# Kernel optimization log

Hardware: AMD Instinct MI355X
Metric: run time of the kernel (lower is better)

The kernel has to match this reference:

```python
import jax, jax.numpy as jnp
import numpy as np

# Model dims (Llama-7B-like with GQA)
HID = 4096      # hidden_size
NH = 32         # query heads
NKV = 8         # kv heads
D = HID // NH   # head_dim = 128
S = 64          # num decode sequences (one token each)
NB = 4096       # num cache blocks
BS = 16         # block size
MC = 1024       # max context length
THETA = 10000.0 # rope base


def _rope(x, positions):
    # x: [S, h, D]; neox-style rotary over full head_dim
    half = D // 2
    inv_freq = 1.0 / (THETA ** (jnp.arange(half, dtype=jnp.float32) * 2.0 / D))
    ang = positions.astype(jnp.float32)[:, None] * inv_freq  # [S, half]
    cos = jnp.cos(ang)[:, None, :]
    sin = jnp.sin(ang)[:, None, :]
    x1, x2 = x[..., :half], x[..., half:]
    return jnp.concatenate([x1 * cos - x2 * sin, x2 * cos + x1 * sin], axis=-1)


def setup_inputs() -> dict:
    key = jax.random.key(0)
    ks = jax.random.split(key, 8)
    hidden_states = jax.random.normal(ks[0], (S, HID), dtype=jnp.float32)
    k_cache = jax.random.normal(ks[1], (NB, BS, NKV, D), dtype=jnp.float32)
    v_cache = jax.random.normal(ks[2], (NB, BS, NKV, D), dtype=jnp.float32)
    qkv_w = jax.random.normal(ks[3], ((NH + 2 * NKV) * D, HID), dtype=jnp.float32) * 0.02
    o_w = jax.random.normal(ks[4], (HID, NH * D), dtype=jnp.float32) * 0.02
    context_lens = jnp.clip(jax.random.randint(ks[5], (S,), 1, MC + 1), 1, MC).astype(jnp.int32)
    positions = (context_lens - 1).astype(jnp.int32)  # current token position
    block_tables = jax.random.randint(ks[6], (S, MC // BS), 0, NB).astype(jnp.int32)
    return {"hidden_states": hidden_states, "k_cache": k_cache, "v_cache": v_cache,
            "qkv_w": qkv_w, "o_w": o_w, "positions": positions,
            "context_lens": context_lens, "block_tables": block_tables}


def reference(hidden_states, k_cache, v_cache, qkv_w, o_w, positions, context_lens, block_tables):
    # QKV projection (no bias)
    qkv = hidden_states @ qkv_w.T  # [S, (NH+2*NKV)*D]
    q, k, v = jnp.split(qkv, [NH * D, NH * D + NKV * D], axis=-1)
    q = _rope(q.reshape(S, NH, D), positions)
    k = _rope(k.reshape(S, NKV, D), positions)
    v = v.reshape(S, NKV, D)

    # paged KV gather via block tables: [S, MC, NKV, D]
    Kg = k_cache[block_tables].reshape(S, MC, NKV, D)
    Vg = v_cache[block_tables].reshape(S, MC, NKV, D)
    # write current token's k/v into its slot (positions = context_len - 1)
    idx = jnp.arange(S)
    Kg = Kg.at[idx, positions].set(k)
    Vg = Vg.at[idx, positions].set(v)

    # GQA attention without expanding KV heads
    G = NH // NKV
    qh = q.reshape(S, NKV, G, D) * (D ** -0.5)
    scores = jnp.einsum('skgd,sckd->skgc', qh, Kg)  # [S, NKV, G, MC]
    mask = jnp.arange(MC)[None, :] < context_lens[:, None]  # [S, MC]
    scores = jnp.where(mask[:, None, None, :], scores, -1e9)
    probs = jax.nn.softmax(scores, axis=-1)
    attn = jnp.einsum('skgc,sckd->skgd', probs, Vg).reshape(S, NH * D)

    # output projection
    return attn @ o_w.T
```

## Files before the change

### kernel.cpp

```cpp
#include <hip/hip_runtime.h>
#include <math.h>

#define HID 4096
#define NH  32
#define NKV 8
#define DH  128
#define SEQ 64
#define BS  16
#define MC  1024
#define QKV_N 6144
#define NPAGES 64
#define KC  64
#define KS  16
#define GQ  4
#define CSPLIT 8
#define TPS 128
#define RT  32
#define NHQ (SEQ * NH)
#define SCALE 0.08838834764831845f

__device__ float g_qkv[SEQ * QKV_N];
__device__ float g_attn[SEQ * HID];
__device__ float g_part[KS * SEQ * QKV_N];
__device__ float g_po[CSPLIT * NHQ * DH];
__device__ float g_pm[CSPLIT * NHQ];
__device__ float g_pl[CSPLIT * NHQ];

__global__ __launch_bounds__(256) void gemm_tile(const float* __restrict__ X,
                                                 const float* __restrict__ W,
                                                 float* __restrict__ P,
                                                 int N, int K) {
    __shared__ float Xs[KC][68];
    __shared__ float Ws[KC][68];
    const int tid = threadIdx.x;
    const int tx = tid & 15;
    const int ty = tid >> 4;
    const int jb = blockIdx.x * 64;
    const int ks = blockIdx.y;
    const int k_lo = ks * (K / KS);
    const int k_hi = k_lo + (K / KS);

    float4 a0 = {0,0,0,0}, a1 = {0,0,0,0}, a2 = {0,0,0,0}, a3 = {0,0,0,0};

    for (int k0 = k_lo; k0 < k_hi; k0 += KC) {
        #pragma unroll
        for (int r = 0; r < 4; ++r) {
            int idx = r * 256 + tid;
            int s  = idx >> 4;
            int k4 = idx & 15;
            float4 v = *(const float4*)(X + (size_t)s * K + k0 + k4 * 4);
            Xs[k4 * 4 + 0][s] = v.x;
            Xs[k4 * 4 + 1][s] = v.y;
            Xs[k4 * 4 + 2][s] = v.z;
            Xs[k4 * 4 + 3][s] = v.w;
        }
        #pragma unroll
        for (int r = 0; r < 4; ++r) {
            int idx = r * 256 + tid;
            int j  = idx >> 4;
            int k4 = idx & 15;
            float4 v = *(const float4*)(W + (size_t)(jb + j) * K + k0 + k4 * 4);
            Ws[k4 * 4 + 0][j] = v.x;
            Ws[k4 * 4 + 1][j] = v.y;
            Ws[k4 * 4 + 2][j] = v.z;
            Ws[k4 * 4 + 3][j] = v.w;
        }
        __syncthreads();
        #pragma unroll
        for (int kk = 0; kk < KC; ++kk) {
            float4 xv = *(const float4*)(&Xs[kk][ty * 4]);
            float4 wv = *(const float4*)(&Ws[kk][tx * 4]);
            a0.x = fmaf(xv.x, wv.x, a0.x); a0.y = fmaf(xv.x, wv.y, a0.y);
            a0.z = fmaf(xv.x, wv.z, a0.z); a0.w = fmaf(xv.x, wv.w, a0.w);
            a1.x = fmaf(xv.y, wv.x, a1.x); a1.y = fmaf(xv.y, wv.y, a1.y);
            a1.z = fmaf(xv.y, wv.z, a1.z); a1.w = fmaf(xv.y, wv.w, a1.w);
            a2.x = fmaf(xv.z, wv.x, a2.x); a2.y = fmaf(xv.z, wv.y, a2.y);
            a2.z = fmaf(xv.z, wv.z, a2.z); a2.w = fmaf(xv.z, wv.w, a2.w);
            a3.x = fmaf(xv.w, wv.x, a3.x); a3.y = fmaf(xv.w, wv.y, a3.y);
            a3.z = fmaf(xv.w, wv.z, a3.z); a3.w = fmaf(xv.w, wv.w, a3.w);
        }
        __syncthreads();
    }
    float* pb = P + (size_t)ks * SEQ * N;
    *(float4*)(pb + (size_t)(ty * 4 + 0) * N + jb + tx * 4) = a0;
    *(float4*)(pb + (size_t)(ty * 4 + 1) * N + jb + tx * 4) = a1;
    *(float4*)(pb + (size_t)(ty * 4 + 2) * N + jb + tx * 4) = a2;
    *(float4*)(pb + (size_t)(ty * 4 + 3) * N + jb + tx * 4) = a3;
}

__global__ __launch_bounds__(256) void reduce_ks(const float* __restrict__ P,
                                                 float* __restrict__ Y, int n4) {
    int t = blockIdx.x * 256 + threadIdx.x;
    if (t >= n4) return;
    const float4* p4 = (const float4*)P;
    float4 r = p4[t];
    #pragma unroll
    for (int i = 1; i < KS; ++i) {
        float4 v = p4[t + (size_t)i * n4];
        r.x += v.x; r.y += v.y; r.z += v.z; r.w += v.w;
    }
    ((float4*)Y)[t] = r;
}

__global__ __launch_bounds__(256) void rope_scalar(float* __restrict__ qkv,
                                                   const int* __restrict__ ia,
                                                   const int* __restrict__ ib) {
    int t = blockIdx.x * 256 + threadIdx.x;
    if (t >= SEQ * (NH + NKV) * 64) return;
    int i = t & 63;
    int h = (t >> 6) % (NH + NKV);
    int s = t / ((NH + NKV) * 64);
    int pos = max(ia[s], ib[s]) - 1;
    float* base = qkv + (size_t)s * QKV_N + (size_t)h * DH;
    float ang = (float)pos / powf(10000.0f, (float)i * 2.0f / (float)DH);
    float sn, c;
    sincosf(ang, &sn, &c);
    float x1 = base[i];
    float x2 = base[i + 64];
    base[i]      = x1 * c - x2 * sn;
    base[i + 64] = x2 * c + x1 * sn;
}

__global__ __launch_bounds__(256) void attn_reg(const float* __restrict__ qkv,
                                                const float* __restrict__ k_cache,
                                                const float* __restrict__ v_cache,
                                                const int* __restrict__ ia,
                                                const int* __restrict__ ib,
                                                const int* __restrict__ block_tables,
                                                float* __restrict__ po,
                                                float* __restrict__ pm,
                                                float* __restrict__ pl) {
    __shared__ float Vlds[2][RT][132];
    __shared__ float sc_lds[2][GQ][34];
    __shared__ int   btl[NPAGES];

    int b  = blockIdx.x;
    int t  = b & 7;
    int kv = (b >> 3) & 7;
    int s  = b >> 6;
    int tid = threadIdx.x;
    int lane = tid & 63;
    int g = tid >> 6;

    int L   = max(ia[s], ib[s]);
    int pos = L - 1;
    int c_lo = t * TPS;
    if (c_lo >= L) return;
    int c_hi = min(c_lo + TPS, L);
    int n = c_hi - c_lo;
    int nrounds = (n + RT - 1) >> 5;

    const int sr = tid >> 3;
    const int sq = tid & 7;

    if (tid < NPAGES) btl[tid] = block_tables[s * NPAGES + tid];
    __syncthreads();

    const float* knew = qkv + (size_t)s * QKV_N + (size_t)NH * DH + (size_t)kv * DH;
    const float* vnew = qkv + (size_t)s * QKV_N + (size_t)(NH + NKV) * DH + (size_t)kv * DH;

    float4 qf[GQ][4];
    #pragma unroll
    for (int gg = 0; gg < GQ; ++gg) {
        const float4* qr = (const float4*)(qkv + (size_t)s * QKV_N
                                           + (size_t)(kv * GQ + gg) * DH);
        #pragma unroll
        for (int j = 0; j < 4; ++j) {
            float4 v = qr[sq + 8 * j];
            v.x *= SCALE; v.y *= SCALE; v.z *= SCALE; v.w *= SCALE;
            qf[gg][j] = v;
        }
    }

    float4 ka0, ka1, ka2, ka3, va0, va1, va2, va3;
    bool vrow;

#define LOADR(BASE) do {                                                        \
    int cc = c_lo + (BASE) + sr;                                                \
    vrow = cc < c_hi;                                                           \
    int cs = vrow ? cc : pos;                                                   \
    const float* kp_ = (cs == pos) ? knew                                       \
        : k_cache + ((size_t)btl[cs >> 4] * BS + (cs & 15)) * (size_t)(NKV * DH)\
                  + (size_t)kv * DH;                                            \
    const float* vp_ = (cs == pos) ? vnew                                       \
        : v_cache + ((size_t)btl[cs >> 4] * BS + (cs & 15)) * (size_t)(NKV * DH)\
                  + (size_t)kv * DH;                                            \
    const float4* kp4_ = (const float4*)kp_;                                    \
    const float4* vp4_ = (const float4*)vp_;                                    \
    ka0 = kp4_[sq];      ka1 = kp4_[sq + 8];                                    \
    ka2 = kp4_[sq + 16]; ka3 = kp4_[sq + 24];                                   \
    va0 = vp4_[sq];      va1 = vp4_[sq + 8];                                    \
    va2 = vp4_[sq + 16]; va3 = vp4_[sq + 24];                                   \
} while (0)

#define DOT4(Q, K) ((Q).x*(K).x + (Q).y*(K).y + (Q).z*(K).z + (Q).w*(K).w)

#define STORER(BUF) do {                                                        \
    float pp0 = DOT4(qf[0][0],ka0)+DOT4(qf[0][1],ka1)                           \
              + DOT4(qf[0][2],ka2)+DOT4(qf[0][3],ka3);                          \
    float pp1 = DOT4(qf[1][0],ka0)+DOT4(qf[1][1],ka1)                           \
              + DOT4(qf[1][2],ka2)+DOT4(qf[1][3],ka3);                          \
    float pp2 = DOT4(qf[2][0],ka0)+DOT4(qf[2][1],ka1)                           \
              + DOT4(qf[2][2],ka2)+DOT4(qf[2][3],ka3);                          \
    float pp3 = DOT4(qf[3][0],ka0)+DOT4(qf[3][1],ka1)                           \
              + DOT4(qf[3][2],ka2)+DOT4(qf[3][3],ka3);                          \
    pp0 += __shfl_xor(pp0, 1, 64); pp0 += __shfl_xor(pp0, 2, 64);               \
    pp0 += __shfl_xor(pp0, 4, 64);                                              \
    pp1 += __shfl_xor(pp1, 1, 64); pp1 += __shfl_xor(pp1, 2, 64);               \
    pp1 += __shfl_xor(pp1, 4, 64);                                              \
    pp2 += __shfl_xor(pp2, 1, 64); pp2 += __shfl_xor(pp2, 2, 64);               \
    pp2 += __shfl_xor(pp2, 4, 64);                                              \
    pp3 += __shfl_xor(pp3, 1, 64); pp3 += __shfl_xor(pp3, 2, 64);               \
    pp3 += __shfl_xor(pp3, 4, 64);                                              \
    if (sq < 4) {                                                               \
        float ppsel = (sq == 0) ? pp0 : (sq == 1) ? pp1 : (sq == 2) ? pp2 : pp3;\
        sc_lds[BUF][sq][sr] = vrow ? ppsel : -1e30f;                            \
    }                                                                           \
    *(float4*)(&Vlds[BUF][sr][4 * sq])        = va0;                            \
    *(float4*)(&Vlds[BUF][sr][4 * (sq + 8)])  = va1;                            \
    *(float4*)(&Vlds[BUF][sr][4 * (sq + 16)]) = va2;                            \
    *(float4*)(&Vlds[BUF][sr][4 * (sq + 24)]) = va3;                            \
} while (0)

    LOADR(0);
    STORER(0);
    __syncthreads();

    float m = -1e30f, l = 0.f, o0 = 0.f, o1 = 0.f;
    int cur = 0;
    const int tkn = lane & 31;

    for (int r = 0; r < nrounds; ++r) {
        int base = r << 5;
        if (r + 1 < nrounds) LOADR(base + RT);

        float sco = sc_lds[cur][g][tkn];
        float rm = sco;
        #pragma unroll
        for (int off = 16; off; off >>= 1) rm = fmaxf(rm, __shfl_xor(rm, off, 64));
        float m_new = fmaxf(m, rm);
        float p = expf(sco - m_new);
        float ps = p;
        #pragma unroll
        for (int off = 16; off; off >>= 1) ps += __shfl_xor(ps, off, 64);
        float rescale = expf(m - m_new);
        l = l * rescale + ps;
        o0 *= rescale; o1 *= rescale;
        m = m_new;

        int cnt = min(RT, n - base);
        for (int j = 0; j < cnt; ++j) {
            float pj = __shfl(p, j, 64);
            float2 v = *(const float2*)(&Vlds[cur][j][2 * lane]);
            o0 = fmaf(pj, v.x, o0);
            o1 = fmaf(pj, v.y, o1);
        }

        if (r + 1 < nrounds) {
            STORER(cur ^ 1);
            __syncthreads();
            cur ^= 1;
        }
    }

    int idx = t * NHQ + s * NH + kv * GQ + g;
    float* ob = po + (size_t)idx * DH;
    ((float2*)ob)[lane] = make_float2(o0, o1);
    if (lane == 0) {
        pm[idx] = m;
        pl[idx] = l;
    }
#undef LOADR
#undef DOT4
#undef STORER
}

__global__ __launch_bounds__(128) void attn_combine(const float* __restrict__ po,
                                                    const float* __restrict__ pm,
                                                    const float* __restrict__ pl,
                                                    const int* __restrict__ ia,
                                                    const int* __restrict__ ib,
                                                    float* __restrict__ attn_out) {
    int sh = blockIdx.x;
    int s  = sh >> 5;
    int d  = threadIdx.x;
    int L  = max(ia[s], ib[s]);
    int nact = (L + TPS - 1) / TPS;
    float mv[CSPLIT];
    float M = -1e30f;
    for (int i = 0; i < nact; ++i) {
        mv[i] = pm[i * NHQ + sh];
        M = fmaxf(M, mv[i]);
    }
    float num = 0.f, denom = 0.f;
    for (int i = 0; i < nact; ++i) {
        float w = expf(mv[i] - M);
        denom += pl[i * NHQ + sh] * w;
        num   += po[(size_t)(i * NHQ + sh) * DH + d] * w;
    }
    attn_out[(size_t)sh * DH + d] = num / denom;
}

extern "C" void kernel_launch(void* const* d_in, const int* in_sizes, int n_in,
                              void* d_out, int out_size, void* d_ws, size_t ws_size,
                              hipStream_t stream) {
    const float *hidden = nullptr, *k_cache = nullptr, *v_cache = nullptr;
    const float *qkv_w = nullptr, *o_w = nullptr;
    const int *i64a = nullptr, *i64b = nullptr, *block_tables = nullptr;
    for (int i = 0; i < n_in; ++i) {
        switch (in_sizes[i]) {
            case SEQ * HID:          hidden = (const float*)d_in[i]; break;
            case 4096 * BS * NKV * DH:
                if (!k_cache) k_cache = (const float*)d_in[i];
                else          v_cache = (const float*)d_in[i];
                break;
            case QKV_N * HID:        qkv_w = (const float*)d_in[i]; break;
            case HID * HID:          o_w   = (const float*)d_in[i]; break;
            case SEQ * NPAGES:       block_tables = (const int*)d_in[i]; break;
            case SEQ:
                if (!i64a) i64a = (const int*)d_in[i];
                else       i64b = (const int*)d_in[i];
                break;
        }
    }
    float* out = (float*)d_out;

    static float* qkv_p  = nullptr;
    static float* attn_p = nullptr;
    static float* part_p = nullptr;
    static float* po_p   = nullptr;
    static float* pm_p   = nullptr;
    static float* pl_p   = nullptr;
    if (!qkv_p) {
        void* p;
        hipGetSymbolAddress(&p, HIP_SYMBOL(g_qkv));  qkv_p  = (float*)p;
        hipGetSymbolAddress(&p, HIP_SYMBOL(g_attn)); attn_p = (float*)p;
        hipGetSymbolAddress(&p, HIP_SYMBOL(g_part)); part_p = (float*)p;
        hipGetSymbolAddress(&p, HIP_SYMBOL(g_po));   po_p   = (float*)p;
        hipGetSymbolAddress(&p, HIP_SYMBOL(g_pm));   pm_p   = (float*)p;
        hipGetSymbolAddress(&p, HIP_SYMBOL(g_pl));   pl_p   = (float*)p;
    }

    gemm_tile<<<dim3(QKV_N / 64, KS), 256, 0, stream>>>(hidden, qkv_w, part_p,
                                                        QKV_N, HID);
    reduce_ks<<<(SEQ * QKV_N / 4 + 255) / 256, 256, 0, stream>>>(part_p, qkv_p,
                                                                 SEQ * QKV_N / 4);
    rope_scalar<<<(SEQ * (NH + NKV) * 64) / 256, 256, 0, stream>>>(qkv_p, i64a, i64b);
    attn_reg<<<SEQ * NKV * CSPLIT, 256, 0, stream>>>(qkv_p, k_cache, v_cache,
                                                     i64a, i64b, block_tables,
                                                     po_p, pm_p, pl_p);
    attn_combine<<<NHQ, 128, 0, stream>>>(po_p, pm_p, pl_p, i64a, i64b, attn_p);
    gemm_tile<<<dim3(HID / 64, KS), 256, 0, stream>>>(attn_p, o_w, part_p,
                                                      HID, HID);
    reduce_ks<<<(SEQ * HID / 4 + 255) / 256, 256, 0, stream>>>(part_p, out,
                                                               SEQ * HID / 4);
}
```

Measured before the change: 206.6 us.

## Replace LDS-tiled GEMM with register-resident X GEMM and vectorize PV accumulation

The shared-memory tiled GEMM is replaced by a kernel in which each lane holds one sequence row of X in registers and reads W rows directly from global memory with wave-uniform (broadcast) loads. The K split drops from 16 to 8, which halves the partial-sum traffic seen by reduce_ks. Separately, the attention PV loop now has each half-wave handle alternate tokens using float4 V reads, followed by a cross-half shuffle reduction, and the V LDS row padding changes. The GEMM change drops the LDS staging and barriers, but it puts more pressure on registers and on the global load path, and it has fewer blocks in flight.

Measured after the change: 825.9 us. 300% more time.

```diff
diff --git a/kernel.cpp b/kernel.cpp
--- a/kernel.cpp
+++ b/kernel.cpp
@@ -10,8 +10,7 @@
 #define MC  1024
 #define QKV_N 6144
 #define NPAGES 64
-#define KC  64
-#define KS  16
+#define KS2 8
 #define GQ  4
 #define CSPLIT 8
 #define TPS 128
@@ -21,71 +20,54 @@
 
 __device__ float g_qkv[SEQ * QKV_N];
 __device__ float g_attn[SEQ * HID];
-__device__ float g_part[KS * SEQ * QKV_N];
+__device__ float g_part[KS2 * SEQ * QKV_N];
 __device__ float g_po[CSPLIT * NHQ * DH];
 __device__ float g_pm[CSPLIT * NHQ];
 __device__ float g_pl[CSPLIT * NHQ];
 
-__global__ __launch_bounds__(256) void gemm_tile(const float* __restrict__ X,
+__global__ __launch_bounds__(256) void gemm_sreg(const float* __restrict__ X,
                                                  const float* __restrict__ W,
                                                  float* __restrict__ P,
                                                  int N, int K) {
-    __shared__ float Xs[KC][68];
-    __shared__ float Ws[KC][68];
-    const int tid = threadIdx.x;
-    const int tx = tid & 15;
-    const int ty = tid >> 4;
-    const int jb = blockIdx.x * 64;
-    const int ks = blockIdx.y;
-    const int k_lo = ks * (K / KS);
-    const int k_hi = k_lo + (K / KS);
-
-    float4 a0 = {0,0,0,0}, a1 = {0,0,0,0}, a2 = {0,0,0,0}, a3 = {0,0,0,0};
-
-    for (int k0 = k_lo; k0 < k_hi; k0 += KC) {
-        #pragma unroll
-        for (int r = 0; r < 4; ++r) {
-            int idx = r * 256 + tid;
-            int s  = idx >> 4;
-            int k4 = idx & 15;
-            float4 v = *(const float4*)(X + (size_t)s * K + k0 + k4 * 4);
-            Xs[k4 * 4 + 0][s] = v.x;
-            Xs[k4 * 4 + 1][s] = v.y;
-            Xs[k4 * 4 + 2][s] = v.z;
-            Xs[k4 * 4 + 3][s] = v.w;
-        }
-        #pragma unroll
-        for (int r = 0; r < 4; ++r) {
-            int idx = r * 256 + tid;
-            int j  = idx >> 4;
-            int k4 = idx & 15;
-            float4 v = *(const float4*)(W + (size_t)(jb + j) * K + k0 + k4 * 4);
-            Ws[k4 * 4 + 0][j] = v.x;
-            Ws[k4 * 4 + 1][j] = v.y;
-            Ws[k4 * 4 + 2][j] = v.z;
-            Ws[k4 * 4 + 3][j] = v.w;
-        }
-        __syncthreads();
-        #pragma unroll
-        for (int kk = 0; kk < KC; ++kk) {
-            float4 xv = *(const float4*)(&Xs[kk][ty * 4]);
-            float4 wv = *(const float4*)(&Ws[kk][tx * 4]);
-            a0.x = fmaf(xv.x, wv.x, a0.x); a0.y = fmaf(xv.x, wv.y, a0.y);
-            a0.z = fmaf(xv.x, wv.z, a0.z); a0.w = fmaf(xv.x, wv.w, a0.w);
-            a1.x = fmaf(xv.y, wv.x, a1.x); a1.y = fmaf(xv.y, wv.y, a1.y);
-            a1.z = fmaf(xv.y, wv.z, a1.z); a1.w = fmaf(xv.y, wv.w, a1.w);
-            a2.x = fmaf(xv.z, wv.x, a2.x); a2.y = fmaf(xv.z, wv.y, a2.y);
-            a2.z = fmaf(xv.z, wv.z, a2.z); a2.w = fmaf(xv.z, wv.w, a2.w);
-            a3.x = fmaf(xv.w, wv.x, a3.x); a3.y = fmaf(xv.w, wv.y, a3.y);
-            a3.z = fmaf(xv.w, wv.z, a3.z); a3.w = fmaf(xv.w, wv.w, a3.w);
-        }
-        __syncthreads();
-    }
-    float* pb = P + (size_t)ks * SEQ * N;
-    *(float4*)(pb + (size_t)(ty * 4 + 0) * N + jb + tx * 4) = a0;
-    *(float4*)(pb + (size_t)(ty * 4 + 1) * N + jb + tx * 4) = a1;
-    *(float4*)(pb + (size_t)(ty * 4 + 2) * N + jb + tx * 4) = a2;
-    *(float4*)(pb + (size_t)(ty * 4 + 3) * N + jb + tx * 4) = a3;
+    const int tid  = threadIdx.x;
+    const int lane = tid & 63;
+    const int w    = tid >> 6;
+    const int jb   = blockIdx.x * 64 + w * 16;
+    const int kspan = K / KS2;
+    const int k_lo  = blockIdx.y * kspan;
+
+    float acc[16];
+    #pragma unroll
+    for (int jj = 0; jj < 16; ++jj) acc[jj] = 0.f;
+
+    for (int kc = 0; kc < kspan; kc += 64) {
+        const int k0 = k_lo + kc;
+        float4 xf[16];
+        const float4* xp = (const float4*)(X + (size_t)lane * K + k0);
+        #pragma unroll
+        for (int i = 0; i < 16; ++i) xf[i] = xp[i];
+
+        #pragma unroll
+        for (int jj = 0; jj < 16; ++jj) {
+            const float4* wp = (const float4*)(W + (size_t)(jb + jj) * K + k0);
+            float a0 = 0.f, a1 = 0.f;
+            #pragma unroll
+            for (int i = 0; i < 16; i += 2) {
+                float4 w0 = wp[i];
+                float4 w1 = wp[i + 1];
+                float4 x0 = xf[i];
+                float4 x1 = xf[i + 1];
+                a0 = fmaf(x0.x, w0.x, a0); a0 = fmaf(x0.y, w0.y, a0);
+                a0 = fmaf(x0.z, w0.z, a0); a0 = fmaf(x0.w, w0.w, a0);
+                a1 = fmaf(x1.x, w1.x, a1); a1 = fmaf(x1.y, w1.y, a1);
+                a1 = fmaf(x1.z, w1.z, a1); a1 = fmaf(x1.w, w1.w, a1);
+            }
+            acc[jj] += a0 + a1;
+        }
+    }
+    float* pb = P + (size_t)blockIdx.y * SEQ * N + (size_t)lane * N + jb;
+    #pragma unroll
+    for (int jj = 0; jj < 16; ++jj) pb[jj] = acc[jj];
 }
 
 __global__ __launch_bounds__(256) void reduce_ks(const float* __restrict__ P,
@@ -95,7 +77,7 @@
     const float4* p4 = (const float4*)P;
     float4 r = p4[t];
     #pragma unroll
-    for (int i = 1; i < KS; ++i) {
+    for (int i = 1; i < KS2; ++i) {
         float4 v = p4[t + (size_t)i * n4];
         r.x += v.x; r.y += v.y; r.z += v.z; r.w += v.w;
     }
@@ -130,7 +112,7 @@
                                                 float* __restrict__ po,
                                                 float* __restrict__ pm,
                                                 float* __restrict__ pl) {
-    __shared__ float Vlds[2][RT][132];
+    __shared__ float Vlds[2][RT][136];
     __shared__ float sc_lds[2][GQ][34];
     __shared__ int   btl[NPAGES];
 
@@ -226,9 +208,12 @@
     STORER(0);
     __syncthreads();
 
-    float m = -1e30f, l = 0.f, o0 = 0.f, o1 = 0.f;
+    float m = -1e30f, l = 0.f;
+    float4 oacc = {0.f, 0.f, 0.f, 0.f};
     int cur = 0;
     const int tkn = lane & 31;
+    const int tg  = lane >> 5;
+    const int dd  = lane & 31;
 
     for (int r = 0; r < nrounds; ++r) {
         int base = r << 5;
@@ -245,15 +230,18 @@
         for (int off = 16; off; off >>= 1) ps += __shfl_xor(ps, off, 64);
         float rescale = expf(m - m_new);
         l = l * rescale + ps;
-        o0 *= rescale; o1 *= rescale;
+        oacc.x *= rescale; oacc.y *= rescale;
+        oacc.z *= rescale; oacc.w *= rescale;
         m = m_new;
 
         int cnt = min(RT, n - base);
-        for (int j = 0; j < cnt; ++j) {
-            float pj = __shfl(p, j, 64);
-            float2 v = *(const float2*)(&Vlds[cur][j][2 * lane]);
-            o0 = fmaf(pj, v.x, o0);
-            o1 = fmaf(pj, v.y, o1);
+        for (int j = 0; j < cnt; j += 2) {
+            float pj = __shfl(p, j + tg, 64);
+            float4 v = *(const float4*)(&Vlds[cur][j + tg][4 * dd]);
+            oacc.x = fmaf(pj, v.x, oacc.x);
+            oacc.y = fmaf(pj, v.y, oacc.y);
+            oacc.z = fmaf(pj, v.z, oacc.z);
+            oacc.w = fmaf(pj, v.w, oacc.w);
         }
 
         if (r + 1 < nrounds) {
@@ -263,9 +251,14 @@
         }
     }
 
+    oacc.x += __shfl_xor(oacc.x, 32, 64);
+    oacc.y += __shfl_xor(oacc.y, 32, 64);
+    oacc.z += __shfl_xor(oacc.z, 32, 64);
+    oacc.w += __shfl_xor(oacc.w, 32, 64);
+
     int idx = t * NHQ + s * NH + kv * GQ + g;
     float* ob = po + (size_t)idx * DH;
-    ((float2*)ob)[lane] = make_float2(o0, o1);
+    if (tg == 0) ((float4*)ob)[dd] = oacc;
     if (lane == 0) {
         pm[idx] = m;
         pl[idx] = l;
@@ -341,8 +334,8 @@
         hipGetSymbolAddress(&p, HIP_SYMBOL(g_pl));   pl_p   = (float*)p;
     }
 
-    gemm_tile<<<dim3(QKV_N / 64, KS), 256, 0, stream>>>(hidden, qkv_w, part_p,
-                                                        QKV_N, HID);
+    gemm_sreg<<<dim3(QKV_N / 64, KS2), 256, 0, stream>>>(hidden, qkv_w, part_p,
+                                                         QKV_N, HID);
     reduce_ks<<<(SEQ * QKV_N / 4 + 255) / 256, 256, 0, stream>>>(part_p, qkv_p,
                                                                  SEQ * QKV_N / 4);
     rope_scalar<<<(SEQ * (NH + NKV) * 64) / 256, 256, 0, stream>>>(qkv_p, i64a, i64b);
@@ -350,8 +343,8 @@
                                                      i64a, i64b, block_tables,
                                                      po_p, pm_p, pl_p);
     attn_combine<<<NHQ, 128, 0, stream>>>(po_p, pm_p, pl_p, i64a, i64b, attn_p);
-    gemm_tile<<<dim3(HID / 64, KS), 256, 0, stream>>>(attn_p, o_w, part_p,
-                                                      HID, HID);
+    gemm_sreg<<<dim3(HID / 64, KS2), 256, 0, stream>>>(attn_p, o_w, part_p,
+                                                       HID, HID);
     reduce_ks<<<(SEQ * HID / 4 + 255) / 256, 256, 0, stream>>>(part_p, out,
                                                                SEQ * HID / 4);
 }
```
